# Optimization experiments

Measured on AMD Instinct MI355X. Metric: run time of the kernel, lower is better.

The kernel has to match this reference:

```python
import jax, jax.numpy as jnp
import numpy as np

SEQ_LEN = 512
JOINT_DIM = 96
DECAY = 0.8


def _predefined_weights(n: int, decay: float) -> np.ndarray:
    # W[i, j] = decay**(i-j) for j <= i, each row normalized to sum 1.
    i = np.arange(n)[:, None]
    j = np.arange(n)[None, :]
    lower = j <= i
    exponent = np.where(lower, i - j, 0)
    w = np.where(lower, decay ** exponent.astype(np.float64), 0.0)
    row_sum = w.sum(axis=1, keepdims=True)
    w = np.where(row_sum > 0, w / row_sum, w)
    return w.astype(np.float32)


def setup_inputs() -> dict:
    key = jax.random.key(0)
    kx, ko = jax.random.split(key)
    x = jax.random.normal(kx, (64, SEQ_LEN, JOINT_DIM), dtype=jnp.float32)
    # learnable parameter (initialized to zeros in the module; small noise for generality)
    learnable_offset = 0.02 * jax.random.normal(ko, (JOINT_DIM, SEQ_LEN, SEQ_LEN), dtype=jnp.float32)
    predefined_weights = jnp.asarray(_predefined_weights(SEQ_LEN, DECAY))
    return {"x": x, "learnable_offset": learnable_offset, "predefined_weights": predefined_weights}


def reference(x, learnable_offset, predefined_weights):
    # masks[j] = softmax(predefined + offset[j], axis=-1)   -> [J, N, N]
    masks = jax.nn.softmax(predefined_weights[None, :, :] + learnable_offset, axis=-1)
    # out[b, n, j] = sum_m masks[j, n, m] * x[b, m, j]      -> [B, N, J]
    return jnp.einsum('jnm,bmj->bnj', masks, x)
```

## Files before the change

kernel.cpp:

```cpp
#include <hip/hip_runtime.h>

#define BATCH 64
#define SEQ   512
#define JDIM  96
#define TN    64
#define KC    64

__global__ __launch_bounds__(256) void transpose_in_kernel(
    const float* __restrict__ x, float* __restrict__ xT) {
  __shared__ float tile[JDIM * 65];
  const int r0 = blockIdx.x * 64;
  const int R = BATCH * SEQ;
  for (int idx = threadIdx.x; idx < 64 * JDIM; idx += 256) {
    int rr = idx / JDIM, j = idx % JDIM;
    tile[j * 65 + rr] = x[(size_t)(r0 + rr) * JDIM + j];
  }
  __syncthreads();
  for (int idx = threadIdx.x; idx < 64 * JDIM; idx += 256) {
    int j = idx / 64, rr = idx % 64;
    xT[(size_t)j * R + r0 + rr] = tile[j * 65 + rr];
  }
}

__global__ __launch_bounds__(256, 4) void fused_kernel(
    const float* __restrict__ xT,
    const float* __restrict__ off,
    const float* __restrict__ pre,
    float* __restrict__ outT) {
  __shared__ float As[BATCH * 65];
  __shared__ float Bs[KC * 68];
  __shared__ float Lred[TN * 17];
  __shared__ float Linv[TN];

  const int j  = blockIdx.x % JDIM;
  const int n0 = (blockIdx.x / JDIM) * TN;

  const int tid = threadIdx.x;
  const int tx = tid & 15;
  const int ty = tid >> 4;

  float Lpart[4] = {0.f, 0.f, 0.f, 0.f};
  float acc[4][4];
#pragma unroll
  for (int i = 0; i < 4; ++i)
#pragma unroll
    for (int q = 0; q < 4; ++q) acc[i][q] = 0.f;

  const float* xTj  = xT  + (size_t)j * (BATCH * SEQ);
  const float* offj = off + (size_t)j * (SEQ * SEQ);

  for (int ch = 0; ch < SEQ / KC; ++ch) {
    const int m0 = ch * KC;
#pragma unroll
    for (int it = 0; it < 4; ++it) {
      const int b = ty + 16 * it;
      float4 v = *(const float4*)(xTj + (size_t)b * SEQ + m0 + 4 * tx);
      const int base = b * 65 + 4 * tx;
      As[base + 0] = v.x; As[base + 1] = v.y; As[base + 2] = v.z; As[base + 3] = v.w;
    }
#pragma unroll
    for (int it = 0; it < 4; ++it) {
      const int nl = ty + 16 * it;
      const int n  = n0 + nl;
      float4 o = *(const float4*)(offj + (size_t)n * SEQ + m0 + 4 * tx);
      float4 p = *(const float4*)(pre  + (size_t)n * SEQ + m0 + 4 * tx);
      const float e0 = __expf(o.x + p.x);
      const float e1 = __expf(o.y + p.y);
      const float e2 = __expf(o.z + p.z);
      const float e3 = __expf(o.w + p.w);
      const int ml = 4 * tx;
      Bs[(ml + 0) * 68 + nl] = e0;
      Bs[(ml + 1) * 68 + nl] = e1;
      Bs[(ml + 2) * 68 + nl] = e2;
      Bs[(ml + 3) * 68 + nl] = e3;
      Lpart[it] += (e0 + e1) + (e2 + e3);
    }
    __syncthreads();
#pragma unroll 8
    for (int k = 0; k < KC; ++k) {
      const float4 bf = *(const float4*)&Bs[k * 68 + 4 * ty];
      const float a0 = As[(4 * tx + 0) * 65 + k];
      const float a1 = As[(4 * tx + 1) * 65 + k];
      const float a2 = As[(4 * tx + 2) * 65 + k];
      const float a3 = As[(4 * tx + 3) * 65 + k];
      acc[0][0] = fmaf(a0, bf.x, acc[0][0]);
      acc[0][1] = fmaf(a0, bf.y, acc[0][1]);
      acc[0][2] = fmaf(a0, bf.z, acc[0][2]);
      acc[0][3] = fmaf(a0, bf.w, acc[0][3]);
      acc[1][0] = fmaf(a1, bf.x, acc[1][0]);
      acc[1][1] = fmaf(a1, bf.y, acc[1][1]);
      acc[1][2] = fmaf(a1, bf.z, acc[1][2]);
      acc[1][3] = fmaf(a1, bf.w, acc[1][3]);
      acc[2][0] = fmaf(a2, bf.x, acc[2][0]);
      acc[2][1] = fmaf(a2, bf.y, acc[2][1]);
      acc[2][2] = fmaf(a2, bf.z, acc[2][2]);
      acc[2][3] = fmaf(a2, bf.w, acc[2][3]);
      acc[3][0] = fmaf(a3, bf.x, acc[3][0]);
      acc[3][1] = fmaf(a3, bf.y, acc[3][1]);
      acc[3][2] = fmaf(a3, bf.z, acc[3][2]);
      acc[3][3] = fmaf(a3, bf.w, acc[3][3]);
    }
    __syncthreads();
  }

#pragma unroll
  for (int it = 0; it < 4; ++it) Lred[(ty + 16 * it) * 17 + tx] = Lpart[it];
  __syncthreads();
  if (tid < TN) {
    float s = 0.f;
#pragma unroll
    for (int i = 0; i < 16; ++i) s += Lred[tid * 17 + i];
    Linv[tid] = 1.0f / s;
  }
  __syncthreads();

  float* outTj = outT + (size_t)j * (SEQ * BATCH);
#pragma unroll
  for (int q = 0; q < 4; ++q) {
    const int n = n0 + 4 * ty + q;
    const float linv = Linv[4 * ty + q];
    float4 v;
    v.x = acc[0][q] * linv;
    v.y = acc[1][q] * linv;
    v.z = acc[2][q] * linv;
    v.w = acc[3][q] * linv;
    *(float4*)(outTj + (size_t)n * BATCH + 4 * tx) = v;
  }
}

__global__ __launch_bounds__(256) void transpose_out_kernel(
    const float* __restrict__ outT, float* __restrict__ out) {
  __shared__ float tile[JDIM * 65];
  const int n = blockIdx.x;
  for (int idx = threadIdx.x; idx < JDIM * BATCH; idx += 256) {
    int j = idx / BATCH, b = idx % BATCH;
    tile[j * 65 + b] = outT[((size_t)j * SEQ + n) * BATCH + b];
  }
  __syncthreads();
  for (int idx = threadIdx.x; idx < JDIM * BATCH; idx += 256) {
    int b = idx / JDIM, j = idx % JDIM;
    out[((size_t)b * SEQ + n) * JDIM + j] = tile[j * 65 + b];
  }
}

extern "C" void kernel_launch(void* const* d_in, const int* in_sizes, int n_in,
                              void* d_out, int out_size, void* d_ws, size_t ws_size,
                              hipStream_t stream) {
  const float* x   = (const float*)d_in[0];
  const float* off = (const float*)d_in[1];
  const float* pre = (const float*)d_in[2];
  float* out = (float*)d_out;

  float* xT   = (float*)d_ws;
  float* outT = xT + (size_t)JDIM * BATCH * SEQ;

  transpose_in_kernel<<<BATCH * SEQ / 64, 256, 0, stream>>>(x, xT);
  fused_kernel<<<JDIM * (SEQ / TN), 256, 0, stream>>>(xT, off, pre, outT);
  transpose_out_kernel<<<SEQ, 256, 0, stream>>>(outT, out);
}
```

Baseline: 211.3 us.

## Use bf16 MFMA for the masked matmul with bf16-packed x and exp tiles

Converts transposed x to bf16 in the input transpose and stores the exponentiated mask tile as bf16 in shared memory. The scalar fp32 FMA inner loop is replaced by 16x16x32 bf16 MFMA instructions, one 32x32 output subtile per wave. This removes the FP32 ALU-bound matmul and halves the xT traffic, but lowers precision to bf16 inputs. The row sums for normalisation stay in fp32.

Result: faster. 178.2 us (-15.6%).

```diff
diff --git a/kernel.cpp b/kernel.cpp
--- a/kernel.cpp
+++ b/kernel.cpp
@@ -5,106 +5,116 @@
 #define JDIM  96
 #define TN    64
 #define KC    64
+#define LDB   72
+
+typedef __attribute__((ext_vector_type(8))) short bf16x8;
+typedef __attribute__((ext_vector_type(4))) float f32x4;
+
+__device__ __forceinline__ unsigned short f2bf(float f) {
+  unsigned u = __float_as_uint(f);
+  u += 0x7FFFu + ((u >> 16) & 1u);
+  return (unsigned short)(u >> 16);
+}
 
 __global__ __launch_bounds__(256) void transpose_in_kernel(
-    const float* __restrict__ x, float* __restrict__ xT) {
+    const float* __restrict__ x, unsigned short* __restrict__ xT) {
   __shared__ float tile[JDIM * 65];
   const int r0 = blockIdx.x * 64;
   const int R = BATCH * SEQ;
   for (int idx = threadIdx.x; idx < 64 * JDIM; idx += 256) {
-    int rr = idx / JDIM, j = idx % JDIM;
+    int rr = idx / JDIM, j = idx - rr * JDIM;
     tile[j * 65 + rr] = x[(size_t)(r0 + rr) * JDIM + j];
   }
   __syncthreads();
-  for (int idx = threadIdx.x; idx < 64 * JDIM; idx += 256) {
-    int j = idx / 64, rr = idx % 64;
-    xT[(size_t)j * R + r0 + rr] = tile[j * 65 + rr];
+  for (int idx = threadIdx.x; idx < JDIM * 32; idx += 256) {
+    int j = idx >> 5, rg = idx & 31;
+    float f0 = tile[j * 65 + 2 * rg];
+    float f1 = tile[j * 65 + 2 * rg + 1];
+    unsigned pk = (unsigned)f2bf(f0) | ((unsigned)f2bf(f1) << 16);
+    *(unsigned*)(&xT[(size_t)j * R + r0 + 2 * rg]) = pk;
   }
 }
 
-__global__ __launch_bounds__(256, 4) void fused_kernel(
-    const float* __restrict__ xT,
+__global__ __launch_bounds__(256, 3) void fused_kernel(
+    const unsigned short* __restrict__ xT,
     const float* __restrict__ off,
     const float* __restrict__ pre,
     float* __restrict__ outT) {
-  __shared__ float As[BATCH * 65];
-  __shared__ float Bs[KC * 68];
+  __shared__ unsigned short As[BATCH * LDB];
+  __shared__ unsigned short Bs[TN * LDB];
   __shared__ float Lred[TN * 17];
   __shared__ float Linv[TN];
 
   const int j  = blockIdx.x % JDIM;
   const int n0 = (blockIdx.x / JDIM) * TN;
 
-  const int tid = threadIdx.x;
-  const int tx = tid & 15;
-  const int ty = tid >> 4;
+  const int tid  = threadIdx.x;
+  const int lane = tid & 63;
+  const int wid  = tid >> 6;
+  const int ln   = lane & 15;
+  const int quad = lane >> 4;
+  const int bw   = (wid & 1) * 32;
+  const int nw   = (wid >> 1) * 32;
 
+  f32x4 acc[2][2];
+#pragma unroll
+  for (int i = 0; i < 2; ++i)
+#pragma unroll
+    for (int q = 0; q < 2; ++q) acc[i][q] = (f32x4){0.f, 0.f, 0.f, 0.f};
   float Lpart[4] = {0.f, 0.f, 0.f, 0.f};
-  float acc[4][4];
-#pragma unroll
-  for (int i = 0; i < 4; ++i)
-#pragma unroll
-    for (int q = 0; q < 4; ++q) acc[i][q] = 0.f;
 
-  const float* xTj  = xT  + (size_t)j * (BATCH * SEQ);
+  const unsigned short* xTj = xT + (size_t)j * (BATCH * SEQ);
   const float* offj = off + (size_t)j * (SEQ * SEQ);
+
+  const int a_kg = tid & 7;
+  const int a_b  = tid >> 3;
+  const int b_mg = tid & 15;
+  const int b_n  = tid >> 4;
 
   for (int ch = 0; ch < SEQ / KC; ++ch) {
     const int m0 = ch * KC;
 #pragma unroll
-    for (int it = 0; it < 4; ++it) {
-      const int b = ty + 16 * it;
-      float4 v = *(const float4*)(xTj + (size_t)b * SEQ + m0 + 4 * tx);
-      const int base = b * 65 + 4 * tx;
-      As[base + 0] = v.x; As[base + 1] = v.y; As[base + 2] = v.z; As[base + 3] = v.w;
+    for (int p = 0; p < 2; ++p) {
+      const int b = a_b + 32 * p;
+      uint4 v = *(const uint4*)(xTj + (size_t)b * SEQ + m0 + 8 * a_kg);
+      *(uint4*)(&As[b * LDB + 8 * a_kg]) = v;
     }
 #pragma unroll
-    for (int it = 0; it < 4; ++it) {
-      const int nl = ty + 16 * it;
-      const int n  = n0 + nl;
-      float4 o = *(const float4*)(offj + (size_t)n * SEQ + m0 + 4 * tx);
-      float4 p = *(const float4*)(pre  + (size_t)n * SEQ + m0 + 4 * tx);
-      const float e0 = __expf(o.x + p.x);
-      const float e1 = __expf(o.y + p.y);
-      const float e2 = __expf(o.z + p.z);
-      const float e3 = __expf(o.w + p.w);
-      const int ml = 4 * tx;
-      Bs[(ml + 0) * 68 + nl] = e0;
-      Bs[(ml + 1) * 68 + nl] = e1;
-      Bs[(ml + 2) * 68 + nl] = e2;
-      Bs[(ml + 3) * 68 + nl] = e3;
-      Lpart[it] += (e0 + e1) + (e2 + e3);
+    for (int p = 0; p < 4; ++p) {
+      const int nl = b_n + 16 * p;
+      const float4 o  = *(const float4*)(offj + (size_t)(n0 + nl) * SEQ + m0 + 4 * b_mg);
+      const float4 pr = *(const float4*)(pre  + (size_t)(n0 + nl) * SEQ + m0 + 4 * b_mg);
+      const float e0 = __expf(o.x + pr.x);
+      const float e1 = __expf(o.y + pr.y);
+      const float e2 = __expf(o.z + pr.z);
+      const float e3 = __expf(o.w + pr.w);
+      Lpart[p] += (e0 + e1) + (e2 + e3);
+      uint2 pk;
+      pk.x = (unsigned)f2bf(e0) | ((unsigned)f2bf(e1) << 16);
+      pk.y = (unsigned)f2bf(e2) | ((unsigned)f2bf(e3) << 16);
+      *(uint2*)(&Bs[nl * LDB + 4 * b_mg]) = pk;
     }
     __syncthreads();
-#pragma unroll 8
-    for (int k = 0; k < KC; ++k) {
-      const float4 bf = *(const float4*)&Bs[k * 68 + 4 * ty];
-      const float a0 = As[(4 * tx + 0) * 65 + k];
-      const float a1 = As[(4 * tx + 1) * 65 + k];
-      const float a2 = As[(4 * tx + 2) * 65 + k];
-      const float a3 = As[(4 * tx + 3) * 65 + k];
-      acc[0][0] = fmaf(a0, bf.x, acc[0][0]);
-      acc[0][1] = fmaf(a0, bf.y, acc[0][1]);
-      acc[0][2] = fmaf(a0, bf.z, acc[0][2]);
-      acc[0][3] = fmaf(a0, bf.w, acc[0][3]);
-      acc[1][0] = fmaf(a1, bf.x, acc[1][0]);
-      acc[1][1] = fmaf(a1, bf.y, acc[1][1]);
-      acc[1][2] = fmaf(a1, bf.z, acc[1][2]);
-      acc[1][3] = fmaf(a1, bf.w, acc[1][3]);
-      acc[2][0] = fmaf(a2, bf.x, acc[2][0]);
-      acc[2][1] = fmaf(a2, bf.y, acc[2][1]);
-      acc[2][2] = fmaf(a2, bf.z, acc[2][2]);
-      acc[2][3] = fmaf(a2, bf.w, acc[2][3]);
-      acc[3][0] = fmaf(a3, bf.x, acc[3][0]);
-      acc[3][1] = fmaf(a3, bf.y, acc[3][1]);
-      acc[3][2] = fmaf(a3, bf.z, acc[3][2]);
-      acc[3][3] = fmaf(a3, bf.w, acc[3][3]);
+#pragma unroll
+    for (int ks = 0; ks < KC; ks += 32) {
+      bf16x8 afrag[2], bfrag[2];
+#pragma unroll
+      for (int i = 0; i < 2; ++i)
+        afrag[i] = *(const bf16x8*)(&As[(bw + 16 * i + ln) * LDB + ks + 8 * quad]);
+#pragma unroll
+      for (int q = 0; q < 2; ++q)
+        bfrag[q] = *(const bf16x8*)(&Bs[(nw + 16 * q + ln) * LDB + ks + 8 * quad]);
+#pragma unroll
+      for (int i = 0; i < 2; ++i)
+#pragma unroll
+        for (int q = 0; q < 2; ++q)
+          acc[i][q] = __builtin_amdgcn_mfma_f32_16x16x32_bf16(afrag[i], bfrag[q], acc[i][q], 0, 0, 0);
     }
     __syncthreads();
   }
 
 #pragma unroll
-  for (int it = 0; it < 4; ++it) Lred[(ty + 16 * it) * 17 + tx] = Lpart[it];
+  for (int p = 0; p < 4; ++p) Lred[(b_n + 16 * p) * 17 + b_mg] = Lpart[p];
   __syncthreads();
   if (tid < TN) {
     float s = 0.f;
@@ -116,15 +126,18 @@
 
   float* outTj = outT + (size_t)j * (SEQ * BATCH);
 #pragma unroll
-  for (int q = 0; q < 4; ++q) {
-    const int n = n0 + 4 * ty + q;
-    const float linv = Linv[4 * ty + q];
-    float4 v;
-    v.x = acc[0][q] * linv;
-    v.y = acc[1][q] * linv;
-    v.z = acc[2][q] * linv;
-    v.w = acc[3][q] * linv;
-    *(float4*)(outTj + (size_t)n * BATCH + 4 * tx) = v;
+  for (int q = 0; q < 2; ++q) {
+    const int nc = nw + 16 * q + ln;
+    const float linv = Linv[nc];
+#pragma unroll
+    for (int i = 0; i < 2; ++i) {
+      float4 v;
+      v.x = acc[i][q][0] * linv;
+      v.y = acc[i][q][1] * linv;
+      v.z = acc[i][q][2] * linv;
+      v.w = acc[i][q][3] * linv;
+      *(float4*)(&outTj[(size_t)(n0 + nc) * BATCH + bw + 16 * i + 4 * quad]) = v;
+    }
   }
 }
 
@@ -133,12 +146,12 @@
   __shared__ float tile[JDIM * 65];
   const int n = blockIdx.x;
   for (int idx = threadIdx.x; idx < JDIM * BATCH; idx += 256) {
-    int j = idx / BATCH, b = idx % BATCH;
+    int j = idx >> 6, b = idx & 63;
     tile[j * 65 + b] = outT[((size_t)j * SEQ + n) * BATCH + b];
   }
   __syncthreads();
   for (int idx = threadIdx.x; idx < JDIM * BATCH; idx += 256) {
-    int b = idx / JDIM, j = idx % JDIM;
+    int b = idx / JDIM, j = idx - b * JDIM;
     out[((size_t)b * SEQ + n) * JDIM + j] = tile[j * 65 + b];
   }
 }
@@ -151,8 +164,8 @@
   const float* pre = (const float*)d_in[2];
   float* out = (float*)d_out;
 
-  float* xT   = (float*)d_ws;
-  float* outT = xT + (size_t)JDIM * BATCH * SEQ;
+  unsigned short* xT = (unsigned short*)d_ws;
+  float* outT = (float*)((char*)d_ws + (size_t)JDIM * BATCH * SEQ * sizeof(unsigned short));
 
   transpose_in_kernel<<<BATCH * SEQ / 64, 256, 0, stream>>>(x, xT);
   fused_kernel<<<JDIM * (SEQ / TN), 256, 0, stream>>>(xT, off, pre, outT);
```
